# Kernel tuning notes

Hardware: AMD Instinct MI355X
Metric: run time of the kernel (lower is better)

## Reference

```python
import jax, jax.numpy as jnp
import numpy as np

H = 32; L = 4; HEADS = 8; VC = 16; BIG = 1e9

def _unit(v):
    return v * jax.lax.rsqrt(jnp.sum(v * v, -1, keepdims=True) + 1e-8)

def _dihedrals(bb):
    n = bb.shape[0]
    X = bb[:, :3].reshape(n * 3, 3)
    U = _unit(X[1:] - X[:-1])
    u2, u1, u0 = U[:-2], U[1:-1], U[2:]
    n2 = _unit(jnp.cross(u2, u1)); n1 = _unit(jnp.cross(u1, u0))
    cosD = jnp.clip(jnp.sum(n2 * n1, -1), -1 + 1e-6, 1 - 1e-6)
    D = jnp.sign(jnp.sum(u2 * n1, -1)) * jnp.arccos(cosD)
    D = jnp.pad(D, (1, 2)).reshape(n, 3)
    return jnp.concatenate([jnp.cos(D), jnp.sin(D)], -1)

def _orientations(x):
    f = jnp.pad(_unit(x[1:] - x[:-1]), ((0, 1), (0, 0)))
    b = jnp.pad(_unit(x[:-1] - x[1:]), ((1, 0), (0, 0)))
    return jnp.stack([f, b], -2)

def _virtual_cb(bb):
    n_, ca, c = bb[:, 0], bb[:, 1], bb[:, 2]
    b = ca - n_; cc = c - ca; a = jnp.cross(b, cc)
    return -0.58273431 * a + 0.56802827 * b - 0.54067466 * cc + ca

def _rbf(d, nbin=16, dmax=20.0):
    mu = jnp.linspace(0.0, dmax, nbin); sig = dmax / nbin
    return jnp.exp(-(((d[..., None] - mu) / sig) ** 2))

def _pos_emb(didx, nemb=16):
    freq = jnp.exp(jnp.arange(0, nemb, 2, dtype=jnp.float32) * (-np.log(10000.0) / nemb))
    ang = didx[..., None].astype(jnp.float32) * freq
    return jnp.concatenate([jnp.cos(ang), jnp.sin(ang)], -1)

def _edge_rot(vec):
    # per-edge rotation aligning edge direction to e_y (equiformer-style)
    nrm = _unit(vec)
    helper = jnp.where(jnp.abs(nrm[..., 2:3]) > 0.99, jnp.array([1.0, 0.0, 0.0]), jnp.array([0.0, 0.0, 1.0]))
    z = _unit(jnp.cross(nrm, helper))
    x = jnp.cross(nrm, z)
    return jnp.stack([x, nrm, z], axis=-2)

def _rot(R, x):
    return jnp.concatenate([x[..., :1, :], jnp.einsum('...ij,...jc->...ic', R, x[..., 1:, :])], -2)

def _rot_inv(R, x):
    return jnp.concatenate([x[..., :1, :], jnp.einsum('...ji,...jc->...ic', R, x[..., 1:, :])], -2)

def _norm_so3(x, g0, b0, g1):
    x0 = x[..., 0, :]; x1 = x[..., 1:, :]
    mu = jnp.mean(x0, -1, keepdims=True)
    var = jnp.var(x0, -1, keepdims=True)
    y0 = (x0 - mu) * jax.lax.rsqrt(var + 1e-6) * g0 + b0
    y1 = x1 * jax.lax.rsqrt(jnp.mean(x1 * x1, (-2, -1), keepdims=True) + 1e-6) * g1
    return jnp.concatenate([y0[..., None, :], y1], -2)

def _project(xin, nbr, R, ef, rw1, rw2, ow):
    src = _rot(R, xin[nbr])                         # [N,k,4,Cin] gather + rotate into edge frame
    rad = jax.nn.silu(ef @ rw1) @ rw2               # [N,k,Cin] radial weights
    msg = _rot_inv(R, src * rad[..., None, :])      # rotate back to global frame
    return jnp.mean(msg, axis=1) @ ow               # [N,4,Cout]

def _forward(bb, latent, ln_g0, ln_b0, ln_g1, bb_rad_w1, bb_rad_w2, bb_out_w,
             lat_rad_w1, lat_rad_w2, lat_out_w, tln_g0, tln_b0, tln_g1,
             attn_w1, attn_w2, v_w, o_w, ffn_w1, ffn_w2, ffn_wg, ffn_v1,
             eu_w1, eu_w2, out_rad_w1, out_rad_w2, out_w,
             seq_w1, seq_b1, seq_w2, seq_b2, seq_w3, seq_b3, x_mask, n_per, k):
    N = bb.shape[0]
    Xca = bb[:, 1]
    # backbone SO3 features [N,4,7]: l=0 dihedrals (padded to 7), l=1 seven vectors
    dih = jnp.pad(_dihedrals(bb), ((0, 0), (0, 1)))
    vecs = jnp.concatenate([bb - Xca[:, None], _orientations(Xca),
                            (_virtual_cb(bb) - Xca)[:, None]], -2)
    bb_feat = jnp.concatenate([dih[:, None, :], jnp.nan_to_num(jnp.swapaxes(vecs, -1, -2))], 1)
    # kNN graph within each chain; masked residues pushed far away
    batch = jnp.arange(N) // n_per
    mx = jnp.where(x_mask[:, None], BIG, Xca)
    sq = jnp.sum(mx * mx, -1)
    d2 = sq[:, None] + sq[None, :] - 2.0 * (mx @ mx.T)
    bad = (batch[:, None] != batch[None, :]) | jnp.eye(N, dtype=bool)
    d2 = jnp.where(bad, BIG, d2)
    _, nbr = jax.lax.top_k(-d2, k)                  # [N,k] source indices per target
    edge_vec = Xca[:, None] - Xca[nbr]
    R = _edge_rot(edge_vec)                         # [N,k,3,3]
    dist = jnp.sqrt(jnp.sum(edge_vec * edge_vec, -1) + 1e-12)
    ef = jnp.concatenate([_rbf(dist), _pos_emb(nbr - jnp.arange(N)[:, None])], -1)  # [N,k,32]
    lat = _norm_so3(latent, ln_g0, ln_b0, ln_g1)
    x = jnp.concatenate([_project(bb_feat, nbr, R, ef, bb_rad_w1, bb_rad_w2, bb_out_w),
                         _project(lat, nbr, R, ef, lat_rad_w1, lat_rad_w2, lat_out_w)], -1)  # [N,4,H]
    for l in range(L):
        xl = _norm_so3(x, tln_g0[l], tln_b0[l], tln_g1[l])
        src = xl[nbr]                               # [N,k,4,H]
        feat = jnp.concatenate([src[..., 0, :],
                                jnp.broadcast_to(xl[:, None, 0, :], src[..., 0, :].shape),
                                ef], -1)            # [N,k,3H]
        alpha = jax.nn.softmax(jax.nn.silu(feat @ attn_w1[l]) @ attn_w2[l], axis=1)  # [N,k,heads]
        v = _rot_inv(R, _rot(R, src) @ v_w[l])      # [N,k,4,heads*vc]
        v = v.reshape(N, k, 4, HEADS, VC)
        agg = jnp.einsum('nkh,nkchv->nchv', alpha, v).reshape(N, 4, HEADS * VC)
        x = x + agg @ o_w[l]
        h = jax.nn.silu(x[:, 0, :] @ ffn_w1[l])
        gate = jax.nn.sigmoid(h @ ffn_wg[l])
        x = x + jnp.concatenate([(h @ ffn_w2[l])[:, None, :],
                                 (x[:, 1:, :] @ ffn_v1[l]) * gate[:, None, :]], 1)
        e_in = jnp.concatenate([ef, x[nbr][..., 0, :],
                                jnp.broadcast_to(x[:, None, 0, :], (N, k, H))], -1)
        ef = ef + jax.nn.silu(e_in @ eu_w1[l]) @ eu_w2[l]
    atoms = _project(x, nbr, R, ef, out_rad_w1, out_rad_w2, out_w)  # [N,4,91]
    decoded_latent = jnp.swapaxes(atoms[:, 1:4, :], -1, -2)         # [N,91,3]
    hh = jax.nn.relu(x[:, 0, :] @ seq_w1 + seq_b1)
    hh = jax.nn.relu(hh @ seq_w2 + seq_b2)
    seq_logits = jax.nn.log_softmax(hh @ seq_w3 + seq_b3, -1)
    return decoded_latent, seq_logits

def setup_inputs() -> dict:
    key = jax.random.key(0)
    N = 8192; n_per = 2048; k = 30
    keys = iter(jax.random.split(key, 64))
    def W(shape):
        fan = shape[-2] if len(shape) > 1 else shape[-1]
        return (jax.random.normal(next(keys), shape) / np.sqrt(fan)).astype(jnp.float32)
    inp = {
        'bb': (jax.random.normal(next(keys), (N, 4, 3)) * 3.0).astype(jnp.float32),
        'latent': jax.random.normal(next(keys), (N, 4, H), dtype=jnp.float32),
        'ln_g0': jnp.ones((H,), jnp.float32), 'ln_b0': jnp.zeros((H,), jnp.float32), 'ln_g1': jnp.ones((H,), jnp.float32),
        'bb_rad_w1': W((H, 64)), 'bb_rad_w2': W((64, 7)), 'bb_out_w': W((7, 16)),
        'lat_rad_w1': W((H, 64)), 'lat_rad_w2': W((64, H)), 'lat_out_w': W((H, 16)),
        'tln_g0': jnp.ones((L, H), jnp.float32), 'tln_b0': jnp.zeros((L, H), jnp.float32), 'tln_g1': jnp.ones((L, H), jnp.float32),
        'attn_w1': W((L, 3 * H, H)), 'attn_w2': W((L, H, HEADS)),
        'v_w': W((L, H, HEADS * VC)), 'o_w': W((L, HEADS * VC, H)),
        'ffn_w1': W((L, H, 2 * H)), 'ffn_w2': W((L, 2 * H, H)), 'ffn_wg': W((L, 2 * H, H)), 'ffn_v1': W((L, H, H)),
        'eu_w1': W((L, 3 * H, 2 * H)), 'eu_w2': W((L, 2 * H, H)),
        'out_rad_w1': W((H, 64)), 'out_rad_w2': W((64, H)), 'out_w': W((H, 91)),
        'seq_w1': W((H, 64)), 'seq_b1': jnp.zeros((64,), jnp.float32),
        'seq_w2': W((64, H)), 'seq_b2': jnp.zeros((H,), jnp.float32),
        'seq_w3': W((H, 20)), 'seq_b3': jnp.zeros((20,), jnp.float32),
        'x_mask': jnp.zeros((N,), bool), 'n_per': n_per, 'k': k,
    }
    return inp

def reference(bb, latent, ln_g0, ln_b0, ln_g1, bb_rad_w1, bb_rad_w2, bb_out_w,
              lat_rad_w1, lat_rad_w2, lat_out_w, tln_g0, tln_b0, tln_g1,
              attn_w1, attn_w2, v_w, o_w, ffn_w1, ffn_w2, ffn_wg, ffn_v1,
              eu_w1, eu_w2, out_rad_w1, out_rad_w2, out_w,
              seq_w1, seq_b1, seq_w2, seq_b2, seq_w3, seq_b3, x_mask, n_per, k):
    return _forward(bb, latent, ln_g0, ln_b0, ln_g1, bb_rad_w1, bb_rad_w2, bb_out_w,
                    lat_rad_w1, lat_rad_w2, lat_out_w, tln_g0, tln_b0, tln_g1,
                    attn_w1, attn_w2, v_w, o_w, ffn_w1, ffn_w2, ffn_wg, ffn_v1,
                    eu_w1, eu_w2, out_rad_w1, out_rad_w2, out_w,
                    seq_w1, seq_b1, seq_w2, seq_b2, seq_w3, seq_b3, x_mask, n_per, k)
```

## Files before the change

kernel.cpp:

```cpp
#include <hip/hip_runtime.h>
#include <math.h>

#define NRES 8192
#define NPER 2048
#define KNB  30
#define NEDGE (NRES*KNB)

typedef float v2f __attribute__((ext_vector_type(2)));

__device__ __forceinline__ float siluf(float x){ return x / (1.0f + __expf(-x)); }
__device__ __forceinline__ v2f splat2(float a){ v2f r; r.x=a; r.y=a; return r; }

__global__ void k_bbfeat(const float* __restrict__ bb, float* __restrict__ bbf,
                         float4* __restrict__ ca){
  int n = blockIdx.x*256 + threadIdx.x;
  if(n >= NRES) return;
  const float* r = bb + n*12;
  float cax=r[3], cay=r[4], caz=r[5];
  ca[n] = make_float4(cax,cay,caz, cax*cax+cay*cay+caz*caz);
  float vx[7],vy[7],vz[7];
  for(int a=0;a<4;a++){ vx[a]=r[a*3]-cax; vy[a]=r[a*3+1]-cay; vz[a]=r[a*3+2]-caz; }
  if(n<NRES-1){
    float dx=bb[(n+1)*12+3]-cax, dy=bb[(n+1)*12+4]-cay, dz=bb[(n+1)*12+5]-caz;
    float s=rsqrtf(dx*dx+dy*dy+dz*dz+1e-8f);
    vx[4]=dx*s; vy[4]=dy*s; vz[4]=dz*s;
  } else { vx[4]=0.f; vy[4]=0.f; vz[4]=0.f; }
  if(n>0){
    float dx=bb[(n-1)*12+3]-cax, dy=bb[(n-1)*12+4]-cay, dz=bb[(n-1)*12+5]-caz;
    float s=rsqrtf(dx*dx+dy*dy+dz*dz+1e-8f);
    vx[5]=dx*s; vy[5]=dy*s; vz[5]=dz*s;
  } else { vx[5]=0.f; vy[5]=0.f; vz[5]=0.f; }
  {
    float bx=cax-r[0], by=cay-r[1], bz=caz-r[2];
    float cx=r[6]-cax, cy=r[7]-cay, cz=r[8]-caz;
    float axx=by*cz-bz*cy, ayy=bz*cx-bx*cz, azz=bx*cy-by*cx;
    vx[6]=-0.58273431f*axx+0.56802827f*bx-0.54067466f*cx;
    vy[6]=-0.58273431f*ayy+0.56802827f*by-0.54067466f*cy;
    vz[6]=-0.58273431f*azz+0.56802827f*bz-0.54067466f*cz;
  }
  float cD[3], sD[3];
  for(int t=0;t<3;t++){
    cD[t]=1.0f; sD[t]=0.0f;
    int f=3*n+t-1;
    if(f>=0 && f<3*NRES-3){
      float X[4][3];
      for(int q=0;q<4;q++){
        int m=f+q, rr=m/3, aa=m-rr*3;
        X[q][0]=bb[rr*12+aa*3]; X[q][1]=bb[rr*12+aa*3+1]; X[q][2]=bb[rr*12+aa*3+2];
      }
      float u2x=X[1][0]-X[0][0], u2y=X[1][1]-X[0][1], u2z=X[1][2]-X[0][2];
      float u1x=X[2][0]-X[1][0], u1y=X[2][1]-X[1][1], u1z=X[2][2]-X[1][2];
      float u0x=X[3][0]-X[2][0], u0y=X[3][1]-X[2][1], u0z=X[3][2]-X[2][2];
      float s2=rsqrtf(u2x*u2x+u2y*u2y+u2z*u2z+1e-8f); u2x*=s2; u2y*=s2; u2z*=s2;
      float s1=rsqrtf(u1x*u1x+u1y*u1y+u1z*u1z+1e-8f); u1x*=s1; u1y*=s1; u1z*=s1;
      float s0=rsqrtf(u0x*u0x+u0y*u0y+u0z*u0z+1e-8f); u0x*=s0; u0y*=s0; u0z*=s0;
      float n2x=u2y*u1z-u2z*u1y, n2y=u2z*u1x-u2x*u1z, n2z=u2x*u1y-u2y*u1x;
      float nn2=rsqrtf(n2x*n2x+n2y*n2y+n2z*n2z+1e-8f); n2x*=nn2; n2y*=nn2; n2z*=nn2;
      float n1x=u1y*u0z-u1z*u0y, n1y=u1z*u0x-u1x*u0z, n1z=u1x*u0y-u1y*u0x;
      float nn1=rsqrtf(n1x*n1x+n1y*n1y+n1z*n1z+1e-8f); n1x*=nn1; n1y*=nn1; n1z*=nn1;
      float dotn = n2x*n1x+n2y*n1y+n2z*n1z;
      float cosD = fminf(fmaxf(dotn, -1.0f+1e-6f), 1.0f-1e-6f);
      float sg = u2x*n1x+u2y*n1y+u2z*n1z;
      if(sg==0.0f){ cD[t]=1.0f; sD[t]=0.0f; }
      else {
        float sgn = (sg>0.0f)?1.0f:-1.0f;
        cD[t]=cosD;
        sD[t]=sgn*sqrtf(fmaxf(1.0f-cosD*cosD,0.0f));
      }
    }
  }
  float* o = bbf + n*28;
  o[0]=cD[0]; o[1]=cD[1]; o[2]=cD[2]; o[3]=sD[0]; o[4]=sD[1]; o[5]=sD[2]; o[6]=0.f;
  for(int c=0;c<7;c++){ o[7+c]=vx[c]; o[14+c]=vy[c]; o[21+c]=vz[c]; }
}

__device__ __forceinline__ unsigned long long knn_extract(const float* __restrict__ vals,
                                                          unsigned &mask, int lane){
  float bm=INFINITY; int ba=0;
  #pragma unroll
  for(int t=0;t<32;t++){
    if(!((mask>>t)&1u) && vals[t]<bm){ bm=vals[t]; ba=t; }
  }
  mask |= 1u<<ba;
  unsigned ub = __float_as_uint(bm);
  ub ^= (ub & 0x80000000u) ? 0xFFFFFFFFu : 0x80000000u;
  return ((unsigned long long)ub<<32) | (unsigned)(ba*64+lane);
}

__global__ __launch_bounds__(256) void k_knn(const float4* __restrict__ ca, int* __restrict__ nbr){
  __shared__ float sx[NPER], sy[NPER], sz[NPER], sq[NPER];
  int wave = threadIdx.x>>6;
  int lane = threadIdx.x&63;
  int i = blockIdx.x*4 + wave;
  int batch = i / NPER;
  int base = batch*NPER;
  for(int t=threadIdx.x; t<NPER; t+=256){
    float4 c = ca[base+t];
    sx[t]=c.x; sy[t]=c.y; sz[t]=c.z; sq[t]=c.w;
  }
  __syncthreads();
  int il = i - base;
  float xi=sx[il], yi=sy[il], zi=sz[il], si=sq[il];
  float vals[32];
  #pragma unroll
  for(int t=0;t<32;t++){
    int j = t*64 + lane;
    float d2 = si + sq[j] - 2.0f*(xi*sx[j]+yi*sy[j]+zi*sz[j]);
    if(j==il) d2 = 1e30f;
    vals[t]=d2;
  }
  unsigned mask = 0;
  unsigned long long s0 = knn_extract(vals, mask, lane);
  unsigned long long s1 = knn_extract(vals, mask, lane);
  unsigned long long s2 = knn_extract(vals, mask, lane);
  unsigned long long s3 = knn_extract(vals, mask, lane);
  const unsigned long long EMPTY = ~0ull;
  for(int it=0; it<KNB; it++){
    unsigned long long m = s0;
    #pragma unroll
    for(int off=32; off>0; off>>=1){
      unsigned long long o = __shfl_xor(m, off, 64);
      m = (o<m) ? o : m;
    }
    if(lane==0) nbr[i*KNB+it] = base + (int)(m & 0x7FFull);
    if((int)(m & 63ull) == lane){
      s0=s1; s1=s2; s2=s3; s3=EMPTY;
      if(s0==EMPTY) s0 = knn_extract(vals, mask, lane);
    }
  }
}

__global__ void k_tbl(float* __restrict__ tbl){
  int i = blockIdx.x*256 + threadIdx.x;
  int d = i>>3, m = i&7;
  float freq = __expf(-1.1512925465f*(float)m);
  float ang = (float)(d-2048)*freq;
  tbl[d*16+m]   = cosf(ang);
  tbl[d*16+8+m] = sinf(ang);
}

__global__ void k_edgefeat(const float4* __restrict__ ca, const int* __restrict__ nbr,
                           const float* __restrict__ tbl, float* __restrict__ ef){
  int e = blockIdx.x*256 + threadIdx.x;
  if(e >= NEDGE) return;
  int n = e/KNB;
  int j = nbr[e];
  float4 cn = ca[n], cj = ca[j];
  float dx=cn.x-cj.x, dy=cn.y-cj.y, dz=cn.z-cj.z;
  float dist = sqrtf(dx*dx+dy*dy+dz*dz + 1e-12f);
  float f[32];
  #pragma unroll
  for(int m=0;m<16;m++){
    float mu = (20.0f/15.0f)*(float)m;
    float t = (dist-mu)*(1.0f/1.25f);
    f[m] = __expf(-t*t);
  }
  {
    const float4* t4 = (const float4*)(tbl + (size_t)(j - n + 2048)*16);
    float4 c0=t4[0], c1=t4[1], s0=t4[2], s1=t4[3];
    f[16]=c0.x; f[17]=c0.y; f[18]=c0.z; f[19]=c0.w;
    f[20]=c1.x; f[21]=c1.y; f[22]=c1.z; f[23]=c1.w;
    f[24]=s0.x; f[25]=s0.y; f[26]=s0.z; f[27]=s0.w;
    f[28]=s1.x; f[29]=s1.y; f[30]=s1.z; f[31]=s1.w;
  }
  float4* o4 = (float4*)(ef + (size_t)e*32);
  #pragma unroll
  for(int q=0;q<8;q++) o4[q] = make_float4(f[q*4],f[q*4+1],f[q*4+2],f[q*4+3]);
}

__global__ void k_norm(const float* __restrict__ in, float* __restrict__ out,
                       const float* __restrict__ g0, const float* __restrict__ b0,
                       const float* __restrict__ g1){
  int tid = blockIdx.x*256 + threadIdx.x;
  int n = tid >> 5, lane = tid & 31;
  if(n >= NRES) return;
  const float* xn = in + n*128;
  float x0 = xn[lane];
  float s = x0, s2 = x0*x0;
  for(int off=16; off>0; off>>=1){ s += __shfl_xor(s, off, 32); s2 += __shfl_xor(s2, off, 32); }
  float mu = s*(1.0f/32.0f);
  float var = s2*(1.0f/32.0f) - mu*mu;
  float y0 = (x0-mu)*rsqrtf(var+1e-6f)*g0[lane] + b0[lane];
  float v1 = xn[32+lane], v2 = xn[64+lane], v3 = xn[96+lane];
  float ss = v1*v1+v2*v2+v3*v3;
  for(int off=16; off>0; off>>=1){ ss += __shfl_xor(ss, off, 32); }
  float sc = rsqrtf(ss*(1.0f/96.0f) + 1e-6f);
  float g = g1[lane];
  out[n*128+lane]     = y0;
  out[n*128+32+lane]  = v1*sc*g;
  out[n*128+64+lane]  = v2*sc*g;
  out[n*128+96+lane]  = v3*sc*g;
}

__device__ __forceinline__ void load32(float* __restrict__ f, const float* __restrict__ src){
  const float4* s4 = (const float4*)src;
  #pragma unroll
  for(int q=0;q<8;q++){
    float4 v = s4[q];
    f[q*4+0]=v.x; f[q*4+1]=v.y; f[q*4+2]=v.z; f[q*4+3]=v.w;
  }
}

__global__ __launch_bounds__(128, 4)
void k_rad(const float* __restrict__ ef,
           const float* __restrict__ bbw1, const float* __restrict__ bbw2,
           const float* __restrict__ latw1, const float* __restrict__ latw2,
           float* __restrict__ radbb, float* __restrict__ radlat){
  int e = blockIdx.x*128 + threadIdx.x;
  float f[32];
  load32(f, ef + (size_t)e*32);
  float ab[7];
  #pragma unroll
  for(int t=0;t<7;t++) ab[t]=0.f;
  #pragma unroll
  for(int half=0; half<2; half++){
    v2f h[16];
    #pragma unroll
    for(int o=0;o<16;o++) h[o]=splat2(0.f);
    #pragma unroll
    for(int c=0;c<32;c++){
      v2f fc = splat2(f[c]);
      const v2f* w = (const v2f*)(bbw1 + c*64 + half*32);
      #pragma unroll
      for(int o=0;o<16;o++) h[o] += fc*w[o];
    }
    #pragma unroll
    for(int o=0;o<16;o++){
      float v0 = siluf(h[o].x), v1 = siluf(h[o].y);
      const float* wa = bbw2 + (half*32+o*2)*7;
      const float* wb = bbw2 + (half*32+o*2+1)*7;
      #pragma unroll
      for(int t=0;t<7;t++) ab[t] += v0*wa[t];
      #pragma unroll
      for(int t=0;t<7;t++) ab[t] += v1*wb[t];
    }
  }
  {
    float4* rb4 = (float4*)(radbb + (size_t)e*8);
    rb4[0] = make_float4(ab[0],ab[1],ab[2],ab[3]);
    rb4[1] = make_float4(ab[4],ab[5],ab[6],0.f);
  }
  v2f al[16];
  #pragma unroll
  for(int t=0;t<16;t++) al[t]=splat2(0.f);
  #pragma unroll
  for(int half=0; half<2; half++){
    v2f h[16];
    #pragma unroll
    for(int o=0;o<16;o++) h[o]=splat2(0.f);
    #pragma unroll
    for(int c=0;c<32;c++){
      v2f fc = splat2(f[c]);
      const v2f* w = (const v2f*)(latw1 + c*64 + half*32);
      #pragma unroll
      for(int o=0;o<16;o++) h[o] += fc*w[o];
    }
    #pragma unroll
    for(int o=0;o<16;o++){
      float v0 = siluf(h[o].x), v1 = siluf(h[o].y);
      const v2f* wa = (const v2f*)(latw2 + (half*32+o*2)*32);
      const v2f* wb = (const v2f*)(latw2 + (half*32+o*2+1)*32);
      v2f va = splat2(v0), vb = splat2(v1);
      #pragma unroll
      for(int t=0;t<16;t++) al[t] += va*wa[t];
      #pragma unroll
      for(int t=0;t<16;t++) al[t] += vb*wb[t];
    }
  }
  v2f* rl2 = (v2f*)(radlat + (size_t)e*32);
  #pragma unroll
  for(int q=0;q<16;q++) rl2[q] = al[q];
}

__global__ __launch_bounds__(256) void k_init(const int* __restrict__ nbr,
                       const float* __restrict__ radbb, const float* __restrict__ radlat,
                       const float* __restrict__ bbf, const float* __restrict__ latn,
                       const float* __restrict__ bboutw, const float* __restrict__ latoutw,
                       const float* __restrict__ g0, const float* __restrict__ b0,
                       const float* __restrict__ g1,
                       float* __restrict__ x, float* __restrict__ xl){
  __shared__ float msgbb[4][32], msglat[4][128], xout[4][128];
  int g = threadIdx.x>>6, t = threadIdx.x&63;
  int n = blockIdx.x*4 + g;
  int t31 = t&31, t7 = t%7;
  float accL0=0.f, accL1=0.f, accB=0.f;
  for(int kk=0; kk<KNB; kk++){
    int e = n*KNB+kk;
    int j = nbr[e];
    float rl = radlat[(size_t)e*32 + t31];
    accL0 += latn[j*128+t]    * rl;
    accL1 += latn[j*128+64+t] * rl;
    if(t<28) accB += bbf[j*28+t]*radbb[(size_t)e*8 + t7];
  }
  msglat[g][t]=accL0*(1.0f/KNB); msglat[g][64+t]=accL1*(1.0f/KNB);
  if(t<28) msgbb[g][t]=accB*(1.0f/KNB);
  for(int half=0; half<2; half++){
    int e = half*64+t;
    int rrow = e>>5, c = e&31;
    float v=0.f;
    if(c<16){ for(int q=0;q<7;q++)  v += msgbb[g][rrow*7+q]*bboutw[q*16+c]; }
    else    { for(int q=0;q<32;q++) v += msglat[g][rrow*32+q]*latoutw[q*16+(c-16)]; }
    xout[g][e]=v;
    x[n*128+e]=v;
  }
  if(t<32){
    float x0=xout[g][t];
    float s=x0, s2=x0*x0;
    for(int off=16; off>0; off>>=1){ s+=__shfl_xor(s,off,32); s2+=__shfl_xor(s2,off,32); }
    float mu=s*(1.0f/32.0f), var=s2*(1.0f/32.0f)-mu*mu;
    float y0=(x0-mu)*rsqrtf(var+1e-6f)*g0[t]+b0[t];
    float v1=xout[g][32+t], v2=xout[g][64+t], v3=xout[g][96+t];
    float ss=v1*v1+v2*v2+v3*v3;
    for(int off=16; off>0; off>>=1) ss+=__shfl_xor(ss,off,32);
    float sc=rsqrtf(ss*(1.0f/96.0f)+1e-6f);
    float gg=g1[t];
    xl[n*128+t]=y0; xl[n*128+32+t]=v1*sc*gg; xl[n*128+64+t]=v2*sc*gg; xl[n*128+96+t]=v3*sc*gg;
  }
}

__global__ __launch_bounds__(256) void k_nodeprep(const float* __restrict__ x,
                       const float* __restrict__ xl,
                       const float* __restrict__ ew1, const float* __restrict__ aw1,
                       float* __restrict__ hsrc, float* __restrict__ hdst,
                       float* __restrict__ asrc, float* __restrict__ adst){
  __shared__ float sx[4][32], sl[4][32];
  int g = threadIdx.x>>6, lane = threadIdx.x&63;
  int n = blockIdx.x*4 + g;
  if(lane<32){
    if(x)   sx[g][lane] = x[n*128+lane];
    if(aw1) sl[g][lane] = xl[n*128+lane];
  }
  __syncthreads();
  if(x){
    float a0=0.f, a1=0.f;
    #pragma unroll
    for(int c=0;c<32;c++){
      float xv = sx[g][c];
      a0 += xv*ew1[(32+c)*64+lane];
      a1 += xv*ew1[(64+c)*64+lane];
    }
    hsrc[n*64+lane]=a0; hdst[n*64+lane]=a1;
  }
  if(aw1){
    int o = lane&31;
    int roff = (lane>=32)? 32 : 0;
    float a=0.f;
    #pragma unroll
    for(int c=0;c<32;c++) a += sl[g][c]*aw1[(roff+c)*32+o];
    if(lane<32) asrc[n*32+o]=a; else adst[n*32+o]=a;
  }
}

__global__ __launch_bounds__(128, 4)
void k_logits(const int* __restrict__ nbr,
              const float* __restrict__ asrc, const float* __restrict__ adst,
              const float* __restrict__ ef, const float* __restrict__ w1,
              const float* __restrict__ w2, float* __restrict__ logits){
  int e = blockIdx.x*128 + threadIdx.x;
  int n = e/KNB;
  int j = nbr[e];
  v2f h[16];
  {
    const v2f* pj = (const v2f*)(asrc + (size_t)j*32);
    const v2f* pn = (const v2f*)(adst + (size_t)n*32);
    #pragma unroll
    for(int q=0;q<16;q++) h[q] = pj[q]+pn[q];
  }
  float f[32];
  load32(f, ef + (size_t)e*32);
  #pragma unroll
  for(int c=0;c<32;c++){
    v2f fc = splat2(f[c]);
    const v2f* w = (const v2f*)(w1 + (64+c)*32);
    #pragma unroll
    for(int o=0;o<16;o++) h[o] += fc*w[o];
  }
  v2f acc[4];
  #pragma unroll
  for(int t=0;t<4;t++) acc[t]=splat2(0.f);
  #pragma unroll
  for(int o=0;o<16;o++){
    float v0 = siluf(h[o].x), v1 = siluf(h[o].y);
    const v2f* wa = (const v2f*)(w2 + (o*2)*8);
    const v2f* wb = (const v2f*)(w2 + (o*2+1)*8);
    v2f va = splat2(v0), vb = splat2(v1);
    #pragma unroll
    for(int t=0;t<4;t++) acc[t] += va*wa[t];
    #pragma unroll
    for(int t=0;t<4;t++) acc[t] += vb*wb[t];
  }
  v2f* lg2 = (v2f*)(logits + (size_t)e*8);
  #pragma unroll
  for(int q=0;q<4;q++) lg2[q] = acc[q];
}

__global__ __launch_bounds__(256) void k_update(const int* __restrict__ nbr, const float* __restrict__ xl,
                         const float* __restrict__ logits, float* __restrict__ x,
                         float* __restrict__ xlout,
                         const float* __restrict__ vw, const float* __restrict__ ow,
                         const float* __restrict__ fw1, const float* __restrict__ fw2,
                         const float* __restrict__ fwg, const float* __restrict__ fv1,
                         const float* __restrict__ g0, const float* __restrict__ b0,
                         const float* __restrict__ g1){
  __shared__ float S_lg[4][240], S_m[4][8], S_inv[4][8];
  __shared__ float S_S[4][1024], S_agg[4][512], S_x[4][128];
  __shared__ float S_h[4][64], S_g[4][32], S_d0[4][32];
  int g = threadIdx.x>>6, t = threadIdx.x&63;
  int n = blockIdx.x*4 + g;
  for(int r=t; r<240; r+=64) S_lg[g][r] = logits[(size_t)n*240+r];
  if(t<8){
    float m=-1e30f;
    for(int kk=0;kk<KNB;kk++) m=fmaxf(m, S_lg[g][kk*8+t]);
    float s=0.f;
    for(int kk=0;kk<KNB;kk++) s += __expf(S_lg[g][kk*8+t]-m);
    S_m[g][t]=m; S_inv[g][t]=1.0f/s;
  }
  for(int r=t; r<240; r+=64){ int h=r&7; S_lg[g][r]=__expf(S_lg[g][r]-S_m[g][h])*S_inv[g][h]; }
  int hd = t>>3, i8 = t&7;
  v2f acc[8];
  #pragma unroll
  for(int m=0;m<8;m++) acc[m]=splat2(0.f);
  for(int kk=0;kk<KNB;kk++){
    int j=nbr[n*KNB+kk];
    v2f a = splat2(S_lg[g][kk*8+hd]);
    const v2f* xr = (const v2f*)(xl + (size_t)j*128 + i8*16);
    #pragma unroll
    for(int q=0;q<8;q++) acc[q] += a*xr[q];
  }
  #pragma unroll
  for(int q=0;q<8;q++){ S_S[g][hd*128 + i8*16 + 2*q] = acc[q].x; S_S[g][hd*128 + i8*16 + 2*q+1] = acc[q].y; }
  __syncthreads();
  for(int half=0; half<2; half++){
    int hv = half*64+t;
    int hh = hv>>4;
    v2f a01=splat2(0.f), a23=splat2(0.f);
    for(int c=0;c<32;c++){
      v2f w = splat2(vw[c*128+hv]);
      v2f s01; s01.x = S_S[g][hh*128 + c];      s01.y = S_S[g][hh*128 + 32+c];
      v2f s23; s23.x = S_S[g][hh*128 + 64+c];   s23.y = S_S[g][hh*128 + 96+c];
      a01 += s01*w; a23 += s23*w;
    }
    S_agg[g][hv]=a01.x; S_agg[g][128+hv]=a01.y; S_agg[g][256+hv]=a23.x; S_agg[g][384+hv]=a23.y;
  }
  __syncthreads();
  {
    int c = t&31, r0 = t>>5;
    v2f v01; v01.x = x[n*128+t]; v01.y = x[n*128+64+t];
    for(int hv=0;hv<128;hv++){
      v2f s; s.x = S_agg[g][r0*128+hv]; s.y = S_agg[g][(r0+2)*128+hv];
      v01 += s*splat2(ow[hv*32+c]);
    }
    S_x[g][t]=v01.x; S_x[g][64+t]=v01.y;
  }
  __syncthreads();
  {
    float hs=0.f;
    for(int c=0;c<32;c++) hs += S_x[g][c]*fw1[c*64+t];
    S_h[g][t]=siluf(hs);
  }
  __syncthreads();
  if(t<32){
    float gs=0.f, d0=0.f;
    for(int c=0;c<64;c++){ float hv=S_h[g][c]; gs += hv*fwg[c*32+t]; d0 += hv*fw2[c*32+t]; }
    S_g[g][t]=1.0f/(1.0f+__expf(-gs));
    S_d0[g][t]=d0;
  }
  __syncthreads();
  for(int half=0; half<2; half++){
    int e = half*64+t;
    int rrow = e>>5, c = e&31;
    float xv = S_x[g][e], outv;
    if(rrow==0){ outv = xv + S_d0[g][c]; }
    else {
      float dv=0.f;
      for(int cc=0;cc<32;cc++) dv += S_x[g][rrow*32+cc]*fv1[cc*32+c];
      outv = xv + dv*S_g[g][c];
    }
    __syncthreads();
    S_x[g][e]=outv;
    x[n*128+e]=outv;
  }
  __syncthreads();
  if(t<32){
    float x0=S_x[g][t];
    float s=x0, s2=x0*x0;
    for(int off=16; off>0; off>>=1){ s+=__shfl_xor(s,off,32); s2+=__shfl_xor(s2,off,32); }
    float mu=s*(1.0f/32.0f), var=s2*(1.0f/32.0f)-mu*mu;
    float y0=(x0-mu)*rsqrtf(var+1e-6f)*g0[t]+b0[t];
    float v1=S_x[g][32+t], v2=S_x[g][64+t], v3=S_x[g][96+t];
    float ss=v1*v1+v2*v2+v3*v3;
    for(int off=16; off>0; off>>=1) ss+=__shfl_xor(ss,off,32);
    float sc=rsqrtf(ss*(1.0f/96.0f)+1e-6f);
    float gg=g1[t];
    xlout[n*128+t]=y0; xlout[n*128+32+t]=v1*sc*gg;
    xlout[n*128+64+t]=v2*sc*gg; xlout[n*128+96+t]=v3*sc*gg;
  }
}

template<bool FUSE_LOGITS>
__global__ __launch_bounds__(128, 4)
void k_efup_t(const int* __restrict__ nbr,
              const float* __restrict__ hsrc, const float* __restrict__ hdst,
              const float* __restrict__ ew1, const float* __restrict__ ew2,
              float* __restrict__ ef,
              const float* __restrict__ asrc, const float* __restrict__ adst,
              const float* __restrict__ aw1n, const float* __restrict__ aw2n,
              float* __restrict__ logits){
  int e = blockIdx.x*128 + threadIdx.x;
  int n = e/KNB;
  int j = nbr[e];
  float f[32];
  load32(f, ef + (size_t)e*32);
  v2f acc[16];
  #pragma unroll
  for(int t=0;t<16;t++) acc[t]=splat2(0.f);
  #pragma unroll
  for(int half=0; half<2; half++){
    v2f h[16];
    {
      const v2f* pj = (const v2f*)(hsrc + (size_t)j*64 + half*32);
      const v2f* pn = (const v2f*)(hdst + (size_t)n*64 + half*32);
      #pragma unroll
      for(int q=0;q<16;q++) h[q] = pj[q]+pn[q];
    }
    #pragma unroll
    for(int c=0;c<32;c++){
      v2f fc = splat2(f[c]);
      const v2f* w = (const v2f*)(ew1 + c*64 + half*32);
      #pragma unroll
      for(int o=0;o<16;o++) h[o] += fc*w[o];
    }
    #pragma unroll
    for(int o=0;o<16;o++){
      float v0 = siluf(h[o].x), v1 = siluf(h[o].y);
      const v2f* wa = (const v2f*)(ew2 + (half*32+o*2)*32);
      const v2f* wb = (const v2f*)(ew2 + (half*32+o*2+1)*32);
      v2f va = splat2(v0), vb = splat2(v1);
      #pragma unroll
      for(int t=0;t<16;t++) acc[t] += va*wa[t];
      #pragma unroll
      for(int t=0;t<16;t++) acc[t] += vb*wb[t];
    }
  }
  #pragma unroll
  for(int t=0;t<16;t++){ f[2*t] += acc[t].x; f[2*t+1] += acc[t].y; }
  float4* e4 = (float4*)(ef + (size_t)e*32);
  #pragma unroll
  for(int q=0;q<8;q++)
    e4[q] = make_float4(f[q*4+0], f[q*4+1], f[q*4+2], f[q*4+3]);
  if(FUSE_LOGITS){
    v2f h2[16];
    {
      const v2f* pj = (const v2f*)(asrc + (size_t)j*32);
      const v2f* pn = (const v2f*)(adst + (size_t)n*32);
      #pragma unroll
      for(int q=0;q<16;q++) h2[q] = pj[q]+pn[q];
    }
    #pragma unroll
    for(int c=0;c<32;c++){
      v2f fc = splat2(f[c]);
      const v2f* w = (const v2f*)(aw1n + (64+c)*32);
      #pragma unroll
      for(int o=0;o<16;o++) h2[o] += fc*w[o];
    }
    v2f a8[4];
    #pragma unroll
    for(int t=0;t<4;t++) a8[t]=splat2(0.f);
    #pragma unroll
    for(int o=0;o<16;o++){
      float v0 = siluf(h2[o].x), v1 = siluf(h2[o].y);
      const v2f* wa = (const v2f*)(aw2n + (o*2)*8);
      const v2f* wb = (const v2f*)(aw2n + (o*2+1)*8);
      v2f va = splat2(v0), vb = splat2(v1);
      #pragma unroll
      for(int t=0;t<4;t++) a8[t] += va*wa[t];
      #pragma unroll
      for(int t=0;t<4;t++) a8[t] += vb*wb[t];
    }
    v2f* lg2 = (v2f*)(logits + (size_t)e*8);
    #pragma unroll
    for(int q=0;q<4;q++) lg2[q] = a8[q];
  }
}

__global__ __launch_bounds__(128, 4)
void k_orad(const float* __restrict__ ef,
            const float* __restrict__ orw1, const float* __restrict__ orw2,
            float* __restrict__ orad){
  int e = blockIdx.x*128 + threadIdx.x;
  float f[32];
  load32(f, ef + (size_t)e*32);
  v2f acc[16];
  #pragma unroll
  for(int t=0;t<16;t++) acc[t]=splat2(0.f);
  #pragma unroll
  for(int half=0; half<2; half++){
    v2f h[16];
    #pragma unroll
    for(int o=0;o<16;o++) h[o]=splat2(0.f);
    #pragma unroll
    for(int c=0;c<32;c++){
      v2f fc = splat2(f[c]);
      const v2f* w = (const v2f*)(orw1 + c*64 + half*32);
      #pragma unroll
      for(int o=0;o<16;o++) h[o] += fc*w[o];
    }
    #pragma unroll
    for(int o=0;o<16;o++){
      float v0 = siluf(h[o].x), v1 = siluf(h[o].y);
      const v2f* wa = (const v2f*)(orw2 + (half*32+o*2)*32);
      const v2f* wb = (const v2f*)(orw2 + (half*32+o*2+1)*32);
      v2f va = splat2(v0), vb = splat2(v1);
      #pragma unroll
      for(int t=0;t<16;t++) acc[t] += va*wa[t];
      #pragma unroll
      for(int t=0;t<16;t++) acc[t] += vb*wb[t];
    }
  }
  v2f* r2 = (v2f*)(orad + (size_t)e*32);
  #pragma unroll
  for(int q=0;q<16;q++) r2[q] = acc[q];
}

__global__ __launch_bounds__(256) void k_out(const int* __restrict__ nbr, const float* __restrict__ orad,
                      const float* __restrict__ x,
                      const float* __restrict__ outw,
                      const float* __restrict__ sw1, const float* __restrict__ sb1,
                      const float* __restrict__ sw2, const float* __restrict__ sb2,
                      const float* __restrict__ sw3, const float* __restrict__ sb3,
                      float* __restrict__ out, float* __restrict__ outseq){
  __shared__ float msg[4][128];
  __shared__ float h1[4][64], h2[4][32], lgs[4][20];
  int g = threadIdx.x>>6, t = threadIdx.x&63;
  int n = blockIdx.x*4 + g;
  int t31 = t&31;
  float acc0=0.f, acc1=0.f;
  for(int kk=0;kk<KNB;kk++){
    int e=n*KNB+kk;
    int j=nbr[e];
    float rl = orad[(size_t)e*32 + t31];
    acc0 += x[j*128+t]*rl;
    acc1 += x[j*128+64+t]*rl;
  }
  msg[g][t]=acc0*(1.0f/KNB); msg[g][64+t]=acc1*(1.0f/KNB);
  for(int o=t;o<91;o+=64){
    for(int rrow=1;rrow<4;rrow++){
      float s=0.f;
      for(int c=0;c<32;c++) s += msg[g][rrow*32+c]*outw[c*91+o];
      out[(size_t)n*273 + o*3 + (rrow-1)] = s;
    }
  }
  {
    float s=0.f;
    for(int c=0;c<32;c++) s += x[n*128+c]*sw1[c*64+t];
    h1[g][t]=fmaxf(s+sb1[t],0.f);
  }
  if(t<32){
    float s=0.f;
    for(int c=0;c<64;c++) s += h1[g][c]*sw2[c*32+t];
    h2[g][t]=fmaxf(s+sb2[t],0.f);
  }
  if(t<20){
    float s=0.f;
    for(int c=0;c<32;c++) s += h2[g][c]*sw3[c*20+t];
    lgs[g][t]=s+sb3[t];
  }
  if(t<20){
    float m=-1e30f;
    for(int c=0;c<20;c++) m=fmaxf(m,lgs[g][c]);
    float se=0.f;
    for(int c=0;c<20;c++) se += __expf(lgs[g][c]-m);
    outseq[(size_t)n*20+t]=lgs[g][t]-m-logf(se);
  }
}

extern "C" void kernel_launch(void* const* d_in, const int* in_sizes, int n_in,
                              void* d_out, int out_size, void* d_ws, size_t ws_size,
                              hipStream_t stream) {
  const float* bb      = (const float*)d_in[0];
  const float* latent  = (const float*)d_in[1];
  const float* ln_g0   = (const float*)d_in[2];
  const float* ln_b0   = (const float*)d_in[3];
  const float* ln_g1   = (const float*)d_in[4];
  const float* bbw1    = (const float*)d_in[5];
  const float* bbw2    = (const float*)d_in[6];
  const float* bboutw  = (const float*)d_in[7];
  const float* latw1   = (const float*)d_in[8];
  const float* latw2   = (const float*)d_in[9];
  const float* latoutw = (const float*)d_in[10];
  const float* tg0     = (const float*)d_in[11];
  const float* tb0     = (const float*)d_in[12];
  const float* tg1     = (const float*)d_in[13];
  const float* aw1     = (const float*)d_in[14];
  const float* aw2     = (const float*)d_in[15];
  const float* vw      = (const float*)d_in[16];
  const float* ow      = (const float*)d_in[17];
  const float* fw1     = (const float*)d_in[18];
  const float* fw2     = (const float*)d_in[19];
  const float* fwg     = (const float*)d_in[20];
  const float* fv1     = (const float*)d_in[21];
  const float* ew1     = (const float*)d_in[22];
  const float* ew2     = (const float*)d_in[23];
  const float* orw1    = (const float*)d_in[24];
  const float* orw2    = (const float*)d_in[25];
  const float* outw    = (const float*)d_in[26];
  const float* sw1     = (const float*)d_in[27];
  const float* sb1     = (const float*)d_in[28];
  const float* sw2     = (const float*)d_in[29];
  const float* sb2     = (const float*)d_in[30];
  const float* sw3     = (const float*)d_in[31];
  const float* sb3     = (const float*)d_in[32];
  float* outp = (float*)d_out;

  int*    nbr    = (int*)d_ws;
  float*  ef     = (float*)((char*)d_ws + 1024*1024);
  float*  xbuf   = ef   + (size_t)NEDGE*32;
  float*  xlA    = xbuf + (size_t)NRES*128;
  float*  xlB    = xlA  + (size_t)NRES*128;
  float*  bbf    = xlB  + (size_t)NRES*128;
  float*  logits = bbf  + (size_t)NRES*28;
  float4* ca     = (float4*)(logits + (size_t)NEDGE*8);
  float*  edgescratch = (float*)(ca + NRES);
  float*  radbb  = logits;
  float*  radlat = edgescratch;
  float*  orad   = edgescratch;
  float*  tbl    = edgescratch;
  float*  hsrc   = edgescratch;
  float*  hdst   = edgescratch + (size_t)NRES*64;
  float*  asrc   = edgescratch + (size_t)NRES*128;
  float*  adst   = edgescratch + (size_t)NRES*128 + (size_t)NRES*32;

  k_bbfeat  <<<NRES/256, 256, 0, stream>>>(bb, bbf, ca);
  k_knn     <<<NRES/4,   256, 0, stream>>>(ca, nbr);
  k_tbl     <<<4096*8/256, 256, 0, stream>>>(tbl);
  k_edgefeat<<<NEDGE/256, 256, 0, stream>>>(ca, nbr, tbl, ef);
  k_norm    <<<NRES*32/256, 256, 0, stream>>>(latent, xlA, ln_g0, ln_b0, ln_g1);
  k_rad     <<<NEDGE/128, 128, 0, stream>>>(ef, bbw1, bbw2, latw1, latw2, radbb, radlat);
  k_init    <<<NRES/4, 256, 0, stream>>>(nbr, radbb, radlat, bbf, xlA,
                                         bboutw, latoutw,
                                         tg0, tb0, tg1,
                                         xbuf, xlB);
  k_nodeprep<<<NRES/4, 256, 0, stream>>>(nullptr, xlB, ew1, aw1, hsrc, hdst, asrc, adst);
  k_logits  <<<NEDGE/128, 128, 0, stream>>>(nbr, asrc, adst, ef, aw1, aw2, logits);
  for(int l=0;l<4;l++){
    const float* xl_in  = (l&1) ? xlA : xlB;
    float*       xl_out = (l&1) ? xlB : xlA;
    int ln = (l+1<4) ? (l+1) : 3;
    k_update <<<NRES/4, 256, 0, stream>>>(nbr, xl_in, logits, xbuf, xl_out,
                                          vw+l*32*128, ow+l*128*32,
                                          fw1+l*32*64, fw2+l*64*32,
                                          fwg+l*64*32, fv1+l*32*32,
                                          tg0+ln*32, tb0+ln*32, tg1+ln*32);
    if(l<3){
      k_nodeprep<<<NRES/4, 256, 0, stream>>>(xbuf, xl_out, ew1+l*96*64, aw1+(l+1)*96*32,
                                             hsrc, hdst, asrc, adst);
      k_efup_t<true><<<NEDGE/128, 128, 0, stream>>>(nbr, hsrc, hdst,
                                                    ew1+l*96*64, ew2+l*64*32, ef,
                                                    asrc, adst,
                                                    aw1+(l+1)*96*32, aw2+(l+1)*32*8, logits);
    } else {
      k_nodeprep<<<NRES/4, 256, 0, stream>>>(xbuf, xl_out, ew1+l*96*64, nullptr,
                                             hsrc, hdst, asrc, adst);
      k_efup_t<false><<<NEDGE/128, 128, 0, stream>>>(nbr, hsrc, hdst,
                                                     ew1+l*96*64, ew2+l*64*32, ef,
                                                     nullptr, nullptr,
                                                     nullptr, nullptr, nullptr);
    }
  }
  k_orad<<<NEDGE/128, 128, 0, stream>>>(ef, orw1, orw2, orad);
  k_out <<<NRES/4, 256, 0, stream>>>(nbr, orad, xbuf, outw,
                                     sw1, sb1, sw2, sb2, sw3, sb3,
                                     outp, outp + (size_t)NRES*273);
}
```

Before: 1.153 ms.

## Split each edge across four lanes using DPP broadcasts in edge-update kernel

```diff
diff --git a/kernel.cpp b/kernel.cpp
--- a/kernel.cpp
+++ b/kernel.cpp
@@ -10,6 +10,11 @@
 
 __device__ __forceinline__ float siluf(float x){ return x / (1.0f + __expf(-x)); }
 __device__ __forceinline__ v2f splat2(float a){ v2f r; r.x=a; r.y=a; return r; }
+
+template<int Q>
+__device__ __forceinline__ float qb(float v){
+  return __int_as_float(__builtin_amdgcn_mov_dpp(__float_as_int(v), Q*0x55, 0xF, 0xF, true));
+}
 
 __global__ void k_bbfeat(const float* __restrict__ bb, float* __restrict__ bbf,
                          float4* __restrict__ ca){
@@ -498,88 +503,104 @@
 }
 
 template<bool FUSE_LOGITS>
-__global__ __launch_bounds__(128, 4)
-void k_efup_t(const int* __restrict__ nbr,
+__global__ __launch_bounds__(256, 4)
+void k_efup_q(const int* __restrict__ nbr,
               const float* __restrict__ hsrc, const float* __restrict__ hdst,
               const float* __restrict__ ew1, const float* __restrict__ ew2,
               float* __restrict__ ef,
               const float* __restrict__ asrc, const float* __restrict__ adst,
               const float* __restrict__ aw1n, const float* __restrict__ aw2n,
               float* __restrict__ logits){
-  int e = blockIdx.x*128 + threadIdx.x;
+  int tid = blockIdx.x*256 + threadIdx.x;
+  int e = tid>>2, p = tid&3;
   int n = e/KNB;
   int j = nbr[e];
-  float f[32];
-  load32(f, ef + (size_t)e*32);
-  v2f acc[16];
-  #pragma unroll
-  for(int t=0;t<16;t++) acc[t]=splat2(0.f);
-  #pragma unroll
-  for(int half=0; half<2; half++){
-    v2f h[16];
+  float fs[8];
+  {
+    const float4* s4 = (const float4*)(ef + (size_t)e*32 + p*8);
+    float4 a=s4[0], b=s4[1];
+    fs[0]=a.x; fs[1]=a.y; fs[2]=a.z; fs[3]=a.w; fs[4]=b.x; fs[5]=b.y; fs[6]=b.z; fs[7]=b.w;
+  }
+  v2f h[8];
+  {
+    const float4* pj = (const float4*)(hsrc + (size_t)j*64 + p*16);
+    const float4* pn = (const float4*)(hdst + (size_t)n*64 + p*16);
+    #pragma unroll
+    for(int q=0;q<4;q++){
+      float4 a=pj[q], b=pn[q];
+      h[2*q]   = (v2f){a.x+b.x, a.y+b.y};
+      h[2*q+1] = (v2f){a.z+b.z, a.w+b.w};
+    }
+  }
+  #define EW1_BLK(CQ) \
+    { _Pragma("unroll") \
+      for(int i=0;i<8;i++){ \
+        v2f fc = splat2(qb<CQ>(fs[i])); \
+        const v2f* w = (const v2f*)(ew1 + (CQ*8+i)*64 + p*16); \
+        _Pragma("unroll") \
+        for(int o=0;o<8;o++) h[o] += fc*w[o]; \
+      } }
+  EW1_BLK(0) EW1_BLK(1) EW1_BLK(2) EW1_BLK(3)
+  #undef EW1_BLK
+  float s[16];
+  #pragma unroll
+  for(int o=0;o<8;o++){ s[2*o]=siluf(h[o].x); s[2*o+1]=siluf(h[o].y); }
+  v2f acc[4];
+  #pragma unroll
+  for(int t=0;t<4;t++) acc[t]=splat2(0.f);
+  #define EW2_BLK(OQ) \
+    { _Pragma("unroll") \
+      for(int i=0;i<16;i++){ \
+        v2f sv = splat2(qb<OQ>(s[i])); \
+        const v2f* w = (const v2f*)(ew2 + (OQ*16+i)*32 + p*8); \
+        _Pragma("unroll") \
+        for(int t=0;t<4;t++) acc[t] += sv*w[t]; \
+      } }
+  EW2_BLK(0) EW2_BLK(1) EW2_BLK(2) EW2_BLK(3)
+  #undef EW2_BLK
+  #pragma unroll
+  for(int t=0;t<4;t++){ fs[2*t] += acc[t].x; fs[2*t+1] += acc[t].y; }
+  {
+    float4* o4 = (float4*)(ef + (size_t)e*32 + p*8);
+    o4[0] = make_float4(fs[0],fs[1],fs[2],fs[3]);
+    o4[1] = make_float4(fs[4],fs[5],fs[6],fs[7]);
+  }
+  if(FUSE_LOGITS){
+    v2f h2[4];
     {
-      const v2f* pj = (const v2f*)(hsrc + (size_t)j*64 + half*32);
-      const v2f* pn = (const v2f*)(hdst + (size_t)n*64 + half*32);
-      #pragma unroll
-      for(int q=0;q<16;q++) h[q] = pj[q]+pn[q];
-    }
-    #pragma unroll
-    for(int c=0;c<32;c++){
-      v2f fc = splat2(f[c]);
-      const v2f* w = (const v2f*)(ew1 + c*64 + half*32);
-      #pragma unroll
-      for(int o=0;o<16;o++) h[o] += fc*w[o];
-    }
-    #pragma unroll
-    for(int o=0;o<16;o++){
-      float v0 = siluf(h[o].x), v1 = siluf(h[o].y);
-      const v2f* wa = (const v2f*)(ew2 + (half*32+o*2)*32);
-      const v2f* wb = (const v2f*)(ew2 + (half*32+o*2+1)*32);
-      v2f va = splat2(v0), vb = splat2(v1);
-      #pragma unroll
-      for(int t=0;t<16;t++) acc[t] += va*wa[t];
-      #pragma unroll
-      for(int t=0;t<16;t++) acc[t] += vb*wb[t];
-    }
-  }
-  #pragma unroll
-  for(int t=0;t<16;t++){ f[2*t] += acc[t].x; f[2*t+1] += acc[t].y; }
-  float4* e4 = (float4*)(ef + (size_t)e*32);
-  #pragma unroll
-  for(int q=0;q<8;q++)
-    e4[q] = make_float4(f[q*4+0], f[q*4+1], f[q*4+2], f[q*4+3]);
-  if(FUSE_LOGITS){
-    v2f h2[16];
-    {
-      const v2f* pj = (const v2f*)(asrc + (size_t)j*32);
-      const v2f* pn = (const v2f*)(adst + (size_t)n*32);
-      #pragma unroll
-      for(int q=0;q<16;q++) h2[q] = pj[q]+pn[q];
-    }
-    #pragma unroll
-    for(int c=0;c<32;c++){
-      v2f fc = splat2(f[c]);
-      const v2f* w = (const v2f*)(aw1n + (64+c)*32);
-      #pragma unroll
-      for(int o=0;o<16;o++) h2[o] += fc*w[o];
-    }
-    v2f a8[4];
-    #pragma unroll
-    for(int t=0;t<4;t++) a8[t]=splat2(0.f);
-    #pragma unroll
-    for(int o=0;o<16;o++){
-      float v0 = siluf(h2[o].x), v1 = siluf(h2[o].y);
-      const v2f* wa = (const v2f*)(aw2n + (o*2)*8);
-      const v2f* wb = (const v2f*)(aw2n + (o*2+1)*8);
-      v2f va = splat2(v0), vb = splat2(v1);
-      #pragma unroll
-      for(int t=0;t<4;t++) a8[t] += va*wa[t];
-      #pragma unroll
-      for(int t=0;t<4;t++) a8[t] += vb*wb[t];
-    }
-    v2f* lg2 = (v2f*)(logits + (size_t)e*8);
-    #pragma unroll
-    for(int q=0;q<4;q++) lg2[q] = a8[q];
+      const float4* pj = (const float4*)(asrc + (size_t)j*32 + p*8);
+      const float4* pn = (const float4*)(adst + (size_t)n*32 + p*8);
+      #pragma unroll
+      for(int q=0;q<2;q++){
+        float4 a=pj[q], b=pn[q];
+        h2[2*q]   = (v2f){a.x+b.x, a.y+b.y};
+        h2[2*q+1] = (v2f){a.z+b.z, a.w+b.w};
+      }
+    }
+    #define AW1_BLK(CQ) \
+      { _Pragma("unroll") \
+        for(int i=0;i<8;i++){ \
+          v2f fc = splat2(qb<CQ>(fs[i])); \
+          const v2f* w = (const v2f*)(aw1n + (64+CQ*8+i)*32 + p*8); \
+          _Pragma("unroll") \
+          for(int o=0;o<4;o++) h2[o] += fc*w[o]; \
+        } }
+    AW1_BLK(0) AW1_BLK(1) AW1_BLK(2) AW1_BLK(3)
+    #undef AW1_BLK
+    float s2[8];
+    #pragma unroll
+    for(int o=0;o<4;o++){ s2[2*o]=siluf(h2[o].x); s2[2*o+1]=siluf(h2[o].y); }
+    v2f a8 = splat2(0.f);
+    #define AW2_BLK(OQ) \
+      { _Pragma("unroll") \
+        for(int i=0;i<8;i++){ \
+          v2f sv = splat2(qb<OQ>(s2[i])); \
+          const v2f* w = (const v2f*)(aw2n + (OQ*8+i)*8 + p*2); \
+          a8 += sv*w[0]; \
+        } }
+    AW2_BLK(0) AW2_BLK(1) AW2_BLK(2) AW2_BLK(3)
+    #undef AW2_BLK
+    *(v2f*)(logits + (size_t)e*8 + p*2) = a8;
   }
 }
 
@@ -754,17 +775,17 @@
     if(l<3){
       k_nodeprep<<<NRES/4, 256, 0, stream>>>(xbuf, xl_out, ew1+l*96*64, aw1+(l+1)*96*32,
                                              hsrc, hdst, asrc, adst);
-      k_efup_t<true><<<NEDGE/128, 128, 0, stream>>>(nbr, hsrc, hdst,
-                                                    ew1+l*96*64, ew2+l*64*32, ef,
-                                                    asrc, adst,
-                                                    aw1+(l+1)*96*32, aw2+(l+1)*32*8, logits);
+      k_efup_q<true><<<NEDGE/64, 256, 0, stream>>>(nbr, hsrc, hdst,
+                                                   ew1+l*96*64, ew2+l*64*32, ef,
+                                                   asrc, adst,
+                                                   aw1+(l+1)*96*32, aw2+(l+1)*32*8, logits);
     } else {
       k_nodeprep<<<NRES/4, 256, 0, stream>>>(xbuf, xl_out, ew1+l*96*64, nullptr,
                                              hsrc, hdst, asrc, adst);
-      k_efup_t<false><<<NEDGE/128, 128, 0, stream>>>(nbr, hsrc, hdst,
-                                                     ew1+l*96*64, ew2+l*64*32, ef,
-                                                     nullptr, nullptr,
-                                                     nullptr, nullptr, nullptr);
+      k_efup_q<false><<<NEDGE/64, 256, 0, stream>>>(nbr, hsrc, hdst,
+                                                    ew1+l*96*64, ew2+l*64*32, ef,
+                                                    nullptr, nullptr,
+                                                    nullptr, nullptr, nullptr);
     }
   }
   k_orad<<<NEDGE/128, 128, 0, stream>>>(ef, orw1, orw2, orad);
```

Result: slower. 1.584 ms (+37.4%).
